# Optimization experiments

Hardware: AMD Instinct MI355X
Metric: run time of the kernel (lower is better)

The kernel has to match this reference:

```python
import jax, jax.numpy as jnp
import numpy as np

V = 100          # atoms per molecule (reactant and every candidate product)
C = 1000         # number of candidate products (B - 1)
E_R = 250        # directed edges in reactant graph
E_P = C * E_R    # total edges over all candidate product graphs
NODE_IN = 82     # WLN atom feature size
EDGE_IN = 6      # WLN bond feature size
H = 128          # node_hidden_feats
N_LAYERS = 3     # num_encode_gnn_layers


def setup_inputs() -> dict:
    key = jax.random.key(0)
    ks = jax.random.split(key, 20)
    # reactant graph edges
    r_src = jax.random.randint(ks[0], (E_R,), 0, V)
    r_dst = jax.random.randint(ks[1], (E_R,), 0, V)
    # candidate product graphs: random edges within each graph, offset per graph
    p_src_local = jax.random.randint(ks[2], (C, E_R), 0, V)
    p_dst_local = jax.random.randint(ks[3], (C, E_R), 0, V)
    offsets = (jnp.arange(C) * V)[:, None]
    p_src = (p_src_local + offsets).reshape(-1)
    p_dst = (p_dst_local + offsets).reshape(-1)

    def rn(k, shape, scale=0.1):
        return jax.random.normal(k, shape, dtype=jnp.float32) * scale

    return dict(
        reactant_node_feats=rn(ks[4], (V, NODE_IN), 1.0),
        reactant_edge_feats=rn(ks[5], (E_R, EDGE_IN), 1.0),
        product_node_feats=rn(ks[6], (C * V, NODE_IN), 1.0),
        product_edge_feats=rn(ks[7], (E_P, EDGE_IN), 1.0),
        candidate_scores=rn(ks[8], (C, 1), 1.0),
        # shared-weight WLN encoder (used for both reactant and products)
        W_proj=rn(ks[9], (NODE_IN, H)), b_proj=jnp.zeros((H,), jnp.float32),
        W_msg=rn(ks[10], (H + EDGE_IN, H)), b_msg=jnp.zeros((H,), jnp.float32),
        W_new=rn(ks[11], (2 * H, H)), b_new=jnp.zeros((H,), jnp.float32),
        # diff WLN (1 layer, no input projection)
        W_msg_d=rn(ks[12], (H + EDGE_IN, H)), b_msg_d=jnp.zeros((H,), jnp.float32),
        W_new_d=rn(ks[13], (2 * H, H)), b_new_d=jnp.zeros((H,), jnp.float32),
        # prediction head
        W_pred1=rn(ks[14], (H, H)), b_pred1=jnp.zeros((H,), jnp.float32),
        W_pred2=rn(ks[15], (H, 1)), b_pred2=jnp.zeros((1,), jnp.float32),
        reactant_src=r_src, reactant_dst=r_dst,
        product_src=p_src, product_dst=p_dst,
    )


def _wln_layers(h, e, src, dst, n_nodes, W_msg, b_msg, W_new, b_new, n_layers):
    # dgllife WLN: message/update MLP weights are SHARED across the n_layers iterations.
    for _ in range(n_layers):
        # per-edge message: ReLU(Linear([h_src ; e]))  -- [E, H]
        m = jax.nn.relu(jnp.concatenate([h[src], e], axis=1) @ W_msg + b_msg)
        # scatter-sum messages to destination nodes -- [N, H]
        agg = jax.ops.segment_sum(m, dst, num_segments=n_nodes)
        # node update: ReLU(Linear([h ; agg]))
        h = jax.nn.relu(jnp.concatenate([h, agg], axis=1) @ W_new + b_new)
    return h


def reference(reactant_node_feats, reactant_edge_feats, product_node_feats,
              product_edge_feats, candidate_scores,
              W_proj, b_proj, W_msg, b_msg, W_new, b_new,
              W_msg_d, b_msg_d, W_new_d, b_new_d,
              W_pred1, b_pred1, W_pred2, b_pred2,
              reactant_src, reactant_dst, product_src, product_dst):
    # encoder WLN (project_in_feats=True, 3 shared-weight layers)
    r = jax.nn.relu(reactant_node_feats @ W_proj + b_proj)
    r = _wln_layers(r, reactant_edge_feats, reactant_src, reactant_dst, V,
                    W_msg, b_msg, W_new, b_new, N_LAYERS)            # [V, H]
    p = jax.nn.relu(product_node_feats @ W_proj + b_proj)
    p = _wln_layers(p, product_edge_feats, product_src, product_dst, C * V,
                    W_msg, b_msg, W_new, b_new, N_LAYERS)            # [C*V, H]
    # node-wise difference against broadcast reactant features
    diff = (p.reshape(C, V, H) - r[None, :, :]).reshape(-1, H)       # [C*V, H]
    # diff WLN (project_in_feats=False, 1 layer)
    d = _wln_layers(diff, product_edge_feats, product_src, product_dst, C * V,
                    W_msg_d, b_msg_d, W_new_d, b_new_d, 1)           # [C*V, H]
    # sum pooling per candidate graph (each graph has exactly V nodes)
    g = d.reshape(C, V, H).sum(axis=1)                               # [C, H]
    # MLP scorer + candidate scores
    return jax.nn.relu(g @ W_pred1 + b_pred1) @ W_pred2 + b_pred2 + candidate_scores
```

## Files before the change

### kernel.cpp

```cpp
#include <hip/hip_runtime.h>
#include <hip/hip_bf16.h>
#include <cstdint>

#define H 128
#define VV 100
#define CC 1000
#define ER_N 250
#define NODE_IN_N 82
#define EDGE_IN_N 6
#define MROWS 112
#define LDA 136
#define NT 1024
#define NP_TOT 100000

typedef short short8 __attribute__((ext_vector_type(8)));
typedef float floatx4 __attribute__((ext_vector_type(4)));
typedef __hip_bfloat16 bf16;

#define PREP_W (27 * 4096)
#define PREP_X (NP_TOT * 48)
__global__ __launch_bounds__(256) void prep_all(
    const float* __restrict__ Wp, const float* __restrict__ Wm,
    const float* __restrict__ Wn, const float* __restrict__ Wmd,
    const float* __restrict__ Wnd, const float* __restrict__ Xp,
    const float* __restrict__ Epe,
    bf16* __restrict__ wfrag, bf16* __restrict__ Xbf, float* __restrict__ Epad) {
  long idx = (long)blockIdx.x * 256 + threadIdx.x;
  if (idx < PREP_W) {
    const float* W;
    int Ksrc;
    long local = idx;
    if (idx < 3 * 4096)       { W = Wp;  Ksrc = NODE_IN_N; }
    else if (idx < 7 * 4096)  { W = Wm;  Ksrc = H;     local -= 3 * 4096; }
    else if (idx < 15 * 4096) { W = Wn;  Ksrc = 2 * H; local -= 7 * 4096; }
    else if (idx < 19 * 4096) { W = Wmd; Ksrc = H;     local -= 15 * 4096; }
    else                      { W = Wnd; Ksrc = 2 * H; local -= 19 * 4096; }
    int j = local & 7, lane = (local >> 3) & 63, nt = (local >> 9) & 7, kc = local >> 12;
    int k = kc * 32 + ((lane >> 4) & 3) * 8 + j;
    int n = nt * 16 + (lane & 15);
    float v = (k < Ksrc) ? W[(size_t)k * H + n] : 0.f;
    wfrag[idx] = __float2bfloat16(v);
    return;
  }
  idx -= PREP_W;
  if (idx < (long)PREP_X) {
    long r = idx / 48;
    int p = (int)(idx - r * 48);
    int c0 = 2 * p;
    float v0 = (c0 < NODE_IN_N) ? Xp[r * NODE_IN_N + c0] : 0.f;
    float v1 = (c0 + 1 < NODE_IN_N) ? Xp[r * NODE_IN_N + c0 + 1] : 0.f;
    __hip_bfloat162 pk;
    pk.x = __float2bfloat16(v0);
    pk.y = __float2bfloat16(v1);
    *(__hip_bfloat162*)&Xbf[r * 96 + c0] = pk;
    return;
  }
  idx -= (long)PREP_X;
  if (idx < (long)NP_TOT * 20) {
    long e = idx >> 3;
    int k = (int)(idx & 7);
    Epad[idx] = (k < EDGE_IN_N) ? Epe[e * EDGE_IN_N + k] : 0.f;
  }
}

template<int CHUNKS>
__device__ __forceinline__ void load_bfrag(short8 b[CHUNKS], const bf16* __restrict__ Wf,
                                           int nt8, int lane) {
#pragma unroll
  for (int kc = 0; kc < CHUNKS; ++kc)
    b[kc] = *(const short8*)(Wf + ((size_t)((kc * 8 + nt8) * 64 + lane)) * 8);
}

template<int CHUNKS>
__device__ __forceinline__ void mfma_mt(floatx4 acc[4], const short8 b[CHUNKS],
                                        const bf16* A, int m0, int mc,
                                        int l16, int quad) {
#pragma unroll
  for (int kc = 0; kc < CHUNKS; ++kc)
#pragma unroll
    for (int mi = 0; mi < 4; ++mi)
      if (mi < mc) {
        short8 a = *(const short8*)(A + ((m0 + mi) * 16 + l16) * LDA + kc * 32 + quad * 8);
        acc[mi] = __builtin_amdgcn_mfma_f32_16x16x32_bf16(a, b[kc], acc[mi], 0, 0, 0);
      }
}

__device__ __forceinline__ void epi(floatx4 acc[4], const float* __restrict__ bias,
                                    bool relu, bf16* Out,
                                    int nt8, int m0, int mc, int quad, int l16) {
  int col = nt8 * 16 + l16;
  float bb = bias[col];
#pragma unroll
  for (int mi = 0; mi < 4; ++mi)
    if (mi < mc)
#pragma unroll
      for (int r = 0; r < 4; ++r) {
        float v = acc[mi][r] + bb;
        if (relu) v = fmaxf(v, 0.f);
        Out[((m0 + mi) * 16 + quad * 4 + r) * LDA + col] = __float2bfloat16(v);
      }
}

__device__ __forceinline__ void zero4(floatx4 acc[4]) {
#pragma unroll
  for (int mi = 0; mi < 4; ++mi) acc[mi] = (floatx4){0.f, 0.f, 0.f, 0.f};
}

__device__ __forceinline__ void gather(const bf16* sT, bf16* sAgg, const float* sEf,
                                       const int* sRowPtr, const int* sEidx,
                                       const float* __restrict__ WmBot,
                                       int q16, int c2) {
  float wb[EDGE_IN_N][2];
#pragma unroll
  for (int k = 0; k < EDGE_IN_N; ++k) {
    float2 w2 = *(const float2*)&WmBot[k * H + 2 * c2];
    wb[k][0] = w2.x;
    wb[k][1] = w2.y;
  }
#pragma unroll
  for (int i = 0; i < 7; ++i) {
    int n = q16 + 16 * i;
    if (n < VV) {
      int p0 = sRowPtr[n], p1 = sRowPtr[n + 1];
      float a0 = 0.f, a1 = 0.f;
      for (int p = p0; p < p1; ++p) {
        int v = sEidx[p];
        int s = v & 127, e = v >> 7;
        uint32_t tt = *(const uint32_t*)&sT[s * LDA + 2 * c2];
        float u0 = __uint_as_float((tt & 0xffffu) << 16);
        float u1 = __uint_as_float((tt >> 16) << 16);
        float4 ea = *(const float4*)&sEf[e * 8];
        float2 eb = *(const float2*)&sEf[e * 8 + 4];
        u0 = fmaf(ea.x, wb[0][0], u0); u1 = fmaf(ea.x, wb[0][1], u1);
        u0 = fmaf(ea.y, wb[1][0], u0); u1 = fmaf(ea.y, wb[1][1], u1);
        u0 = fmaf(ea.z, wb[2][0], u0); u1 = fmaf(ea.z, wb[2][1], u1);
        u0 = fmaf(ea.w, wb[3][0], u0); u1 = fmaf(ea.w, wb[3][1], u1);
        u0 = fmaf(eb.x, wb[4][0], u0); u1 = fmaf(eb.x, wb[4][1], u1);
        u0 = fmaf(eb.y, wb[5][0], u0); u1 = fmaf(eb.y, wb[5][1], u1);
        a0 += fmaxf(u0, 0.f);
        a1 += fmaxf(u1, 0.f);
      }
      __hip_bfloat162 pk;
      pk.x = __float2bfloat16(a0);
      pk.y = __float2bfloat16(a1);
      *(__hip_bfloat162*)&sAgg[n * LDA + 2 * c2] = pk;
    }
  }
}

__device__ __forceinline__ void wln_layer(
    bf16* sH, bf16* sT, bf16* sAgg, const float* sEf,
    const int* sRowPtr, const int* sEidx,
    const bf16* __restrict__ wf_msg, const float* __restrict__ bmsg,
    const float* __restrict__ WmBot,
    const bf16* __restrict__ wf_new, const float* __restrict__ bnew,
    int lane, int nt8, int m0, int mc, int quad, int l16, int q16, int c2) {
  short8 bm_[4], bu1[4], bu2[4];
  floatx4 accM[4], accU[4];
  load_bfrag<4>(bm_, wf_msg, nt8, lane);
  zero4(accM);
  mfma_mt<4>(accM, bm_, sH, m0, mc, l16, quad);
  load_bfrag<4>(bu1, wf_new, nt8, lane);
  epi(accM, bmsg, false, sT, nt8, m0, mc, quad, l16);
  __syncthreads();
  zero4(accU);
  mfma_mt<4>(accU, bu1, sH, m0, mc, l16, quad);
  load_bfrag<4>(bu2, wf_new + 4 * 4096, nt8, lane);
  gather(sT, sAgg, sEf, sRowPtr, sEidx, WmBot, q16, c2);
  __syncthreads();
  mfma_mt<4>(accU, bu2, sAgg, m0, mc, l16, quad);
  epi(accU, bnew, true, sH, nt8, m0, mc, quad, l16);
  __syncthreads();
}

template<bool PRODUCT>
__global__ __launch_bounds__(NT, 4) void wln_fused(
    const void* __restrict__ Xin, const void* __restrict__ EFin,
    const int* __restrict__ SRC, const int* __restrict__ DST,
    const bf16* __restrict__ wf_proj, const float* __restrict__ bproj,
    const bf16* __restrict__ wf_msg, const float* __restrict__ bmsg,
    const float* __restrict__ WmBot,
    const bf16* __restrict__ wf_new, const float* __restrict__ bnew,
    const bf16* __restrict__ wf_msgd, const float* __restrict__ bmsgd,
    const float* __restrict__ WmdBot,
    const bf16* __restrict__ wf_newd, const float* __restrict__ bnewd,
    bf16* __restrict__ hr_global,
    const float* __restrict__ W1, const float* __restrict__ b1,
    const float* __restrict__ W2, const float* __restrict__ b2,
    const float* __restrict__ scores, float* __restrict__ out) {
  __shared__ bf16 sH[MROWS * LDA];
  __shared__ bf16 sT[MROWS * LDA];
  __shared__ bf16 sAgg[MROWS * LDA];
  __shared__ float sEf[ER_N * 8];
  __shared__ int sRowPtr[VV + 1];
  __shared__ int sCnt[VV];
  __shared__ int sScan[128];
  __shared__ int sSD[ER_N];
  __shared__ int sEidx[ER_N];
  __shared__ float sRed[NT];
  __shared__ float sG[H];

  const int tid = threadIdx.x;
  const int lane = tid & 63;
  const int wave = tid >> 6;
  const int quad = (lane >> 4) & 3, l16 = lane & 15;
  const int nt8 = wave & 7, mh = wave >> 3;
  const int m0 = mh * 4, mc = mh ? 3 : 4;
  const int q16 = tid >> 6, c2 = tid & 63;
  const int c = blockIdx.x;
  const int no = c * VV;
  const long eo = (long)c * ER_N;

  if (tid < VV) sCnt[tid] = 0;
  __syncthreads();
  if (tid < ER_N) {
    int s = SRC[eo + tid] - no;
    int d = DST[eo + tid] - no;
    sSD[tid] = (d << 16) | s;
    atomicAdd(&sCnt[d], 1);
  }
  if (PRODUCT) {
    const float4* Ep = (const float4*)((const float*)EFin + eo * 8);
    for (int f = tid; f < 500; f += NT) ((float4*)sEf)[f] = Ep[f];
    const bf16* Xb = (const bf16*)Xin + (size_t)no * 96;
    for (int f = tid; f < 1200; f += NT) {
      int r = f / 12, g = f - r * 12;
      *(float4*)&sT[r * LDA + g * 8] = *(const float4*)(Xb + r * 96 + g * 8);
    }
  } else {
    const float* Ef = (const float*)EFin;
    for (int f = tid; f < ER_N * EDGE_IN_N; f += NT) {
      int e = f / EDGE_IN_N, k = f - e * EDGE_IN_N;
      sEf[e * 8 + k] = Ef[f];
    }
    const float* X = (const float*)Xin;
    for (int f = tid; f < VV * 96; f += NT) {
      int r = f / 96, cc = f - r * 96;
      float v = (cc < NODE_IN_N) ? X[r * NODE_IN_N + cc] : 0.f;
      sT[r * LDA + cc] = __float2bfloat16(v);
    }
  }
  __syncthreads();
  int myc = 0;
  if (tid < 128) {
    myc = (tid < VV) ? sCnt[tid] : 0;
    sScan[tid] = myc;
  }
  __syncthreads();
  for (int off = 1; off < 128; off <<= 1) {
    int x = (tid < 128 && tid >= off) ? sScan[tid - off] : 0;
    __syncthreads();
    if (tid < 128) sScan[tid] += x;
    __syncthreads();
  }
  if (tid < VV) {
    int ex = sScan[tid] - myc;
    sRowPtr[tid] = ex;
    sCnt[tid] = ex;
  }
  if (tid == 0) sRowPtr[VV] = ER_N;
  __syncthreads();
  if (tid < ER_N) {
    int sd = sSD[tid];
    int p = atomicAdd(&sCnt[sd >> 16], 1);
    sEidx[p] = (sd & 0xffff) | (tid << 7);
  }
  __syncthreads();

  {
    short8 bp_[3];
    floatx4 acc[4];
    load_bfrag<3>(bp_, wf_proj, nt8, lane);
    zero4(acc);
    mfma_mt<3>(acc, bp_, sT, m0, mc, l16, quad);
    epi(acc, bproj, true, sH, nt8, m0, mc, quad, l16);
  }
  __syncthreads();

  for (int l = 0; l < 3; ++l)
    wln_layer(sH, sT, sAgg, sEf, sRowPtr, sEidx, wf_msg, bmsg, WmBot, wf_new, bnew,
              lane, nt8, m0, mc, quad, l16, q16, c2);

  if (!PRODUCT) {
    for (int f = tid; f < VV * H; f += NT)
      hr_global[f] = sH[(f >> 7) * LDA + (f & 127)];
    return;
  }

  for (int f = tid; f < VV * H; f += NT) {
    int r = f >> 7, j = f & 127;
    float v = __bfloat162float(sH[r * LDA + j]) - __bfloat162float(hr_global[f]);
    sH[r * LDA + j] = __float2bfloat16(v);
  }
  __syncthreads();

  wln_layer(sH, sT, sAgg, sEf, sRowPtr, sEidx, wf_msgd, bmsgd, WmdBot, wf_newd, bnewd,
            lane, nt8, m0, mc, quad, l16, q16, c2);

  {
    int j = tid & 127, qq = tid >> 7;
    int start = qq * 12 + ((qq < 4) ? qq : 4);
    int cnt = (qq < 4) ? 13 : 12;
    float p = 0.f;
    for (int v = start; v < start + cnt; ++v)
      p += __bfloat162float(sH[v * LDA + j]);
    sRed[tid] = p;
  }
  __syncthreads();
  if (tid < H) {
    float s = 0.f;
#pragma unroll
    for (int q = 0; q < 8; ++q) s += sRed[q * 128 + tid];
    sG[tid] = s;
  }
  __syncthreads();
  {
    int j = tid & 127, qq = tid >> 7;
    float a = 0.f;
    for (int k = qq * 16; k < qq * 16 + 16; ++k)
      a = fmaf(sG[k], W1[(size_t)k * H + j], a);
    sRed[tid] = a;
  }
  __syncthreads();
  if (tid < H) {
    float m = b1[tid];
#pragma unroll
    for (int q = 0; q < 8; ++q) m += sRed[q * 128 + tid];
    sG[tid] = fmaxf(m, 0.f) * W2[tid];
  }
  __syncthreads();
  for (int s2 = 64; s2 > 0; s2 >>= 1) {
    if (tid < s2) sG[tid] += sG[tid + s2];
    __syncthreads();
  }
  if (tid == 0) out[c] = sG[0] + b2[0] + scores[c];
}

extern "C" void kernel_launch(void* const* d_in, const int* in_sizes, int n_in,
                              void* d_out, int out_size, void* d_ws, size_t ws_size,
                              hipStream_t stream) {
  const float* Xr  = (const float*)d_in[0];
  const float* Ere = (const float*)d_in[1];
  const float* Xp  = (const float*)d_in[2];
  const float* Epe = (const float*)d_in[3];
  const float* sc  = (const float*)d_in[4];
  const float* Wp  = (const float*)d_in[5];
  const float* bp  = (const float*)d_in[6];
  const float* Wm  = (const float*)d_in[7];
  const float* bm  = (const float*)d_in[8];
  const float* Wn  = (const float*)d_in[9];
  const float* bn  = (const float*)d_in[10];
  const float* Wmd = (const float*)d_in[11];
  const float* bmd = (const float*)d_in[12];
  const float* Wnd = (const float*)d_in[13];
  const float* bnd = (const float*)d_in[14];
  const float* W1  = (const float*)d_in[15];
  const float* b1  = (const float*)d_in[16];
  const float* W2  = (const float*)d_in[17];
  const float* b2  = (const float*)d_in[18];
  const int* rsrc  = (const int*)d_in[19];
  const int* rdst  = (const int*)d_in[20];
  const int* psrc  = (const int*)d_in[21];
  const int* pdst  = (const int*)d_in[22];

  bf16* wf_proj = (bf16*)d_ws;
  bf16* wf_msg  = wf_proj + 3 * 4096;
  bf16* wf_new  = wf_msg + 4 * 4096;
  bf16* wf_msgd = wf_new + 8 * 4096;
  bf16* wf_newd = wf_msgd + 4 * 4096;
  bf16* hr      = wf_newd + 8 * 4096;
  bf16* Xbf     = hr + VV * H;
  float* Epad   = (float*)(Xbf + (size_t)NP_TOT * 96);

  float* out = (float*)d_out;

  {
    long total = (long)PREP_W + (long)PREP_X + (long)NP_TOT * 20;
    int blocks = (int)((total + 255) / 256);
    prep_all<<<blocks, 256, 0, stream>>>(Wp, Wm, Wn, Wmd, Wnd, Xp, Epe,
                                         wf_proj, Xbf, Epad);
  }

  wln_fused<false><<<1, NT, 0, stream>>>(
      Xr, Ere, rsrc, rdst, wf_proj, bp, wf_msg, bm, Wm + H * H, wf_new, bn,
      wf_msgd, bmd, Wmd + H * H, wf_newd, bnd, hr, W1, b1, W2, b2, sc, out);
  wln_fused<true><<<CC, NT, 0, stream>>>(
      Xbf, Epad, psrc, pdst, wf_proj, bp, wf_msg, bm, Wm + H * H, wf_new, bn,
      wf_msgd, bmd, Wmd + H * H, wf_newd, bnd, hr, W1, b1, W2, b2, sc, out);
}
```

Before: 306.7 us.

## Cut LDS to two ping-pong buffers and use wave-shuffle scan/reduction

Shared memory drops from three 112-row activation buffers to two 100-row buffers that swap roles each layer, with the aggregation written into the input buffer after an extra barrier. The epilogue skips padding rows, and the launch bound asks for 8 waves per SIMD instead of 4. The shared-memory prefix scan and the final tree reduction become wave-level shuffles, which removes many __syncthreads. The aim is to fit two 1024-thread blocks per CU, at the cost of an extra barrier per layer and a tighter register budget that could cause spills.

New measurement: 449.5 us. 46.6% more time.

```diff
diff --git a/kernel.cpp b/kernel.cpp
--- a/kernel.cpp
+++ b/kernel.cpp
@@ -8,7 +8,6 @@
 #define ER_N 250
 #define NODE_IN_N 82
 #define EDGE_IN_N 6
-#define MROWS 112
 #define LDA 136
 #define NT 1024
 #define NP_TOT 100000
@@ -16,6 +15,17 @@
 typedef short short8 __attribute__((ext_vector_type(8)));
 typedef float floatx4 __attribute__((ext_vector_type(4)));
 typedef __hip_bfloat16 bf16;
+
+#define OFF_B0 0
+#define OFF_B1 27200
+#define OFF_EF 54400
+#define OFF_RP 62400
+#define OFF_CNT 62816
+#define OFF_SD 63216
+#define OFF_EIDX 64216
+#define OFF_RED 65216
+#define OFF_G 69312
+#define SMEM_TOTAL 69824
 
 #define PREP_W (27 * 4096)
 #define PREP_X (NP_TOT * 48)
@@ -95,9 +105,12 @@
     if (mi < mc)
 #pragma unroll
       for (int r = 0; r < 4; ++r) {
-        float v = acc[mi][r] + bb;
-        if (relu) v = fmaxf(v, 0.f);
-        Out[((m0 + mi) * 16 + quad * 4 + r) * LDA + col] = __float2bfloat16(v);
+        int row = (m0 + mi) * 16 + quad * 4 + r;
+        if (row < VV) {
+          float v = acc[mi][r] + bb;
+          if (relu) v = fmaxf(v, 0.f);
+          Out[row * LDA + col] = __float2bfloat16(v);
+        }
       }
 }
 
@@ -106,7 +119,7 @@
   for (int mi = 0; mi < 4; ++mi) acc[mi] = (floatx4){0.f, 0.f, 0.f, 0.f};
 }
 
-__device__ __forceinline__ void gather(const bf16* sT, bf16* sAgg, const float* sEf,
+__device__ __forceinline__ void gather(const bf16* Y, bf16* X, const float* sEf,
                                        const int* sRowPtr, const int* sEidx,
                                        const float* __restrict__ WmBot,
                                        int q16, int c2) {
@@ -126,7 +139,7 @@
       for (int p = p0; p < p1; ++p) {
         int v = sEidx[p];
         int s = v & 127, e = v >> 7;
-        uint32_t tt = *(const uint32_t*)&sT[s * LDA + 2 * c2];
+        uint32_t tt = *(const uint32_t*)&Y[s * LDA + 2 * c2];
         float u0 = __uint_as_float((tt & 0xffffu) << 16);
         float u1 = __uint_as_float((tt >> 16) << 16);
         float4 ea = *(const float4*)&sEf[e * 8];
@@ -143,14 +156,13 @@
       __hip_bfloat162 pk;
       pk.x = __float2bfloat16(a0);
       pk.y = __float2bfloat16(a1);
-      *(__hip_bfloat162*)&sAgg[n * LDA + 2 * c2] = pk;
+      *(__hip_bfloat162*)&X[n * LDA + 2 * c2] = pk;
     }
   }
 }
 
 __device__ __forceinline__ void wln_layer(
-    bf16* sH, bf16* sT, bf16* sAgg, const float* sEf,
-    const int* sRowPtr, const int* sEidx,
+    bf16* X, bf16* Y, const float* sEf, const int* sRowPtr, const int* sEidx,
     const bf16* __restrict__ wf_msg, const float* __restrict__ bmsg,
     const float* __restrict__ WmBot,
     const bf16* __restrict__ wf_new, const float* __restrict__ bnew,
@@ -159,22 +171,23 @@
   floatx4 accM[4], accU[4];
   load_bfrag<4>(bm_, wf_msg, nt8, lane);
   zero4(accM);
-  mfma_mt<4>(accM, bm_, sH, m0, mc, l16, quad);
+  mfma_mt<4>(accM, bm_, X, m0, mc, l16, quad);
   load_bfrag<4>(bu1, wf_new, nt8, lane);
-  epi(accM, bmsg, false, sT, nt8, m0, mc, quad, l16);
+  epi(accM, bmsg, false, Y, nt8, m0, mc, quad, l16);
   __syncthreads();
   zero4(accU);
-  mfma_mt<4>(accU, bu1, sH, m0, mc, l16, quad);
+  mfma_mt<4>(accU, bu1, X, m0, mc, l16, quad);
   load_bfrag<4>(bu2, wf_new + 4 * 4096, nt8, lane);
-  gather(sT, sAgg, sEf, sRowPtr, sEidx, WmBot, q16, c2);
-  __syncthreads();
-  mfma_mt<4>(accU, bu2, sAgg, m0, mc, l16, quad);
-  epi(accU, bnew, true, sH, nt8, m0, mc, quad, l16);
+  __syncthreads();
+  gather(Y, X, sEf, sRowPtr, sEidx, WmBot, q16, c2);
+  __syncthreads();
+  mfma_mt<4>(accU, bu2, X, m0, mc, l16, quad);
+  epi(accU, bnew, true, Y, nt8, m0, mc, quad, l16);
   __syncthreads();
 }
 
 template<bool PRODUCT>
-__global__ __launch_bounds__(NT, 4) void wln_fused(
+__global__ __launch_bounds__(NT, 8) void wln_fused(
     const void* __restrict__ Xin, const void* __restrict__ EFin,
     const int* __restrict__ SRC, const int* __restrict__ DST,
     const bf16* __restrict__ wf_proj, const float* __restrict__ bproj,
@@ -188,17 +201,16 @@
     const float* __restrict__ W1, const float* __restrict__ b1,
     const float* __restrict__ W2, const float* __restrict__ b2,
     const float* __restrict__ scores, float* __restrict__ out) {
-  __shared__ bf16 sH[MROWS * LDA];
-  __shared__ bf16 sT[MROWS * LDA];
-  __shared__ bf16 sAgg[MROWS * LDA];
-  __shared__ float sEf[ER_N * 8];
-  __shared__ int sRowPtr[VV + 1];
-  __shared__ int sCnt[VV];
-  __shared__ int sScan[128];
-  __shared__ int sSD[ER_N];
-  __shared__ int sEidx[ER_N];
-  __shared__ float sRed[NT];
-  __shared__ float sG[H];
+  __shared__ __align__(16) char smem[SMEM_TOTAL];
+  bf16* sB0 = (bf16*)(smem + OFF_B0);
+  bf16* sB1 = (bf16*)(smem + OFF_B1);
+  float* sEf = (float*)(smem + OFF_EF);
+  int* sRowPtr = (int*)(smem + OFF_RP);
+  int* sCnt = (int*)(smem + OFF_CNT);
+  int* sSD = (int*)(smem + OFF_SD);
+  int* sEidx = (int*)(smem + OFF_EIDX);
+  float* sRed = (float*)(smem + OFF_RED);
+  float* sG = (float*)(smem + OFF_G);
 
   const int tid = threadIdx.x;
   const int lane = tid & 63;
@@ -225,7 +237,7 @@
     const bf16* Xb = (const bf16*)Xin + (size_t)no * 96;
     for (int f = tid; f < 1200; f += NT) {
       int r = f / 12, g = f - r * 12;
-      *(float4*)&sT[r * LDA + g * 8] = *(const float4*)(Xb + r * 96 + g * 8);
+      *(float4*)&sB0[r * LDA + g * 8] = *(const float4*)(Xb + r * 96 + g * 8);
     }
   } else {
     const float* Ef = (const float*)EFin;
@@ -237,28 +249,37 @@
     for (int f = tid; f < VV * 96; f += NT) {
       int r = f / 96, cc = f - r * 96;
       float v = (cc < NODE_IN_N) ? X[r * NODE_IN_N + cc] : 0.f;
-      sT[r * LDA + cc] = __float2bfloat16(v);
-    }
-  }
-  __syncthreads();
-  int myc = 0;
-  if (tid < 128) {
-    myc = (tid < VV) ? sCnt[tid] : 0;
-    sScan[tid] = myc;
-  }
-  __syncthreads();
-  for (int off = 1; off < 128; off <<= 1) {
-    int x = (tid < 128 && tid >= off) ? sScan[tid - off] : 0;
-    __syncthreads();
-    if (tid < 128) sScan[tid] += x;
-    __syncthreads();
-  }
-  if (tid < VV) {
-    int ex = sScan[tid] - myc;
-    sRowPtr[tid] = ex;
-    sCnt[tid] = ex;
-  }
-  if (tid == 0) sRowPtr[VV] = ER_N;
+      sB0[r * LDA + cc] = __float2bfloat16(v);
+    }
+  }
+  __syncthreads();
+
+  if (wave == 0) {
+    int c0 = sCnt[lane];
+    int c1 = (lane + 64 < VV) ? sCnt[lane + 64] : 0;
+    int v = c0;
+#pragma unroll
+    for (int d = 1; d < 64; d <<= 1) {
+      int t = __shfl_up(v, d, 64);
+      if (lane >= d) v += t;
+    }
+    int total0 = __shfl(v, 63, 64);
+    int w = c1;
+#pragma unroll
+    for (int d = 1; d < 64; d <<= 1) {
+      int t = __shfl_up(w, d, 64);
+      if (lane >= d) w += t;
+    }
+    int ex0 = v - c0;
+    int ex1 = total0 + w - c1;
+    sRowPtr[lane] = ex0;
+    sCnt[lane] = ex0;
+    if (lane + 64 < VV) {
+      sRowPtr[lane + 64] = ex1;
+      sCnt[lane + 64] = ex1;
+    }
+    if (lane == 0) sRowPtr[VV] = ER_N;
+  }
   __syncthreads();
   if (tid < ER_N) {
     int sd = sSD[tid];
@@ -272,30 +293,36 @@
     floatx4 acc[4];
     load_bfrag<3>(bp_, wf_proj, nt8, lane);
     zero4(acc);
-    mfma_mt<3>(acc, bp_, sT, m0, mc, l16, quad);
-    epi(acc, bproj, true, sH, nt8, m0, mc, quad, l16);
-  }
-  __syncthreads();
-
-  for (int l = 0; l < 3; ++l)
-    wln_layer(sH, sT, sAgg, sEf, sRowPtr, sEidx, wf_msg, bmsg, WmBot, wf_new, bnew,
+    mfma_mt<3>(acc, bp_, sB0, m0, mc, l16, quad);
+    epi(acc, bproj, true, sB1, nt8, m0, mc, quad, l16);
+  }
+  __syncthreads();
+
+  bf16* Hb = sB1;
+  bf16* Tb = sB0;
+
+  for (int l = 0; l < 3; ++l) {
+    wln_layer(Hb, Tb, sEf, sRowPtr, sEidx, wf_msg, bmsg, WmBot, wf_new, bnew,
               lane, nt8, m0, mc, quad, l16, q16, c2);
+    bf16* tmp = Hb; Hb = Tb; Tb = tmp;
+  }
 
   if (!PRODUCT) {
     for (int f = tid; f < VV * H; f += NT)
-      hr_global[f] = sH[(f >> 7) * LDA + (f & 127)];
+      hr_global[f] = Hb[(f >> 7) * LDA + (f & 127)];
     return;
   }
 
   for (int f = tid; f < VV * H; f += NT) {
     int r = f >> 7, j = f & 127;
-    float v = __bfloat162float(sH[r * LDA + j]) - __bfloat162float(hr_global[f]);
-    sH[r * LDA + j] = __float2bfloat16(v);
-  }
-  __syncthreads();
-
-  wln_layer(sH, sT, sAgg, sEf, sRowPtr, sEidx, wf_msgd, bmsgd, WmdBot, wf_newd, bnewd,
+    float v = __bfloat162float(Hb[r * LDA + j]) - __bfloat162float(hr_global[f]);
+    Hb[r * LDA + j] = __float2bfloat16(v);
+  }
+  __syncthreads();
+
+  wln_layer(Hb, Tb, sEf, sRowPtr, sEidx, wf_msgd, bmsgd, WmdBot, wf_newd, bnewd,
             lane, nt8, m0, mc, quad, l16, q16, c2);
+  { bf16* tmp = Hb; Hb = Tb; Tb = tmp; }
 
   {
     int j = tid & 127, qq = tid >> 7;
@@ -303,7 +330,7 @@
     int cnt = (qq < 4) ? 13 : 12;
     float p = 0.f;
     for (int v = start; v < start + cnt; ++v)
-      p += __bfloat162float(sH[v * LDA + j]);
+      p += __bfloat162float(Hb[v * LDA + j]);
     sRed[tid] = p;
   }
   __syncthreads();
@@ -329,11 +356,12 @@
     sG[tid] = fmaxf(m, 0.f) * W2[tid];
   }
   __syncthreads();
-  for (int s2 = 64; s2 > 0; s2 >>= 1) {
-    if (tid < s2) sG[tid] += sG[tid + s2];
-    __syncthreads();
-  }
-  if (tid == 0) out[c] = sG[0] + b2[0] + scores[c];
+  if (wave == 0) {
+    float v = sG[lane] + sG[lane + 64];
+#pragma unroll
+    for (int d = 32; d > 0; d >>= 1) v += __shfl_down(v, d, 64);
+    if (lane == 0) out[c] = v + b2[0] + scores[c];
+  }
 }
 
 extern "C" void kernel_launch(void* const* d_in, const int* in_sizes, int n_in,
```
